# Performance work log

Measured on AMD Instinct MI355X. Metric: run time of the kernel, lower is better.

Reference implementation:

```python
import jax, jax.numpy as jnp
import numpy as np

N = 50000
F_DIM = 128
H_DIM = 128
E = 800000


def setup_inputs() -> dict:
    key = jax.random.key(0)
    ks = jax.random.split(key, 8)
    x = jax.random.normal(ks[0], (N, F_DIM), dtype=jnp.float32)
    edge_weight = jax.random.uniform(ks[1], (E,), dtype=jnp.float32)
    src = jax.random.randint(ks[2], (E,), 0, N)
    dst = jax.random.randint(ks[3], (E,), 0, N)
    edge_index = jnp.stack([src, dst]).astype(jnp.int64)
    sc = 1.0 / np.sqrt(F_DIM)
    W1 = jax.random.normal(ks[4], (F_DIM, H_DIM), dtype=jnp.float32) * sc
    W2 = jax.random.normal(ks[5], (H_DIM, H_DIM), dtype=jnp.float32) * sc
    Wfc = jax.random.normal(ks[6], (H_DIM, F_DIM), dtype=jnp.float32) * sc
    b1 = jnp.zeros((H_DIM,), jnp.float32)
    b2 = jnp.zeros((H_DIM,), jnp.float32)
    bfc = jnp.zeros((F_DIM,), jnp.float32)
    return {"x": x, "edge_weight": edge_weight, "W1": W1, "b1": b1,
            "W2": W2, "b2": b2, "Wfc": Wfc, "bfc": bfc,
            "edge_index": edge_index}


def _gcn_norm(src, dst, edge_weight, num_nodes):
    # PyG gcn_norm: add self-loops (weight 1), symmetric D^-1/2 A D^-1/2
    loop = jnp.arange(num_nodes, dtype=src.dtype)
    src2 = jnp.concatenate([src, loop])
    dst2 = jnp.concatenate([dst, loop])
    w2 = jnp.concatenate([edge_weight, jnp.ones((num_nodes,), edge_weight.dtype)])
    deg = jax.ops.segment_sum(w2, dst2, num_segments=num_nodes)
    dinv = jnp.where(deg > 0, jax.lax.rsqrt(jnp.where(deg > 0, deg, 1.0)), 0.0)
    norm = dinv[src2] * w2 * dinv[dst2]
    return src2, dst2, norm


def _gcn_conv(x, W, b, src, dst, norm, num_nodes):
    h = x @ W                              # [N, out]
    msg = norm[:, None] * h[src]           # gather + scale, [E+N, out]
    agg = jax.ops.segment_sum(msg, dst, num_segments=num_nodes)
    return agg + b


def reference(x, edge_weight, W1, b1, W2, b2, Wfc, bfc, edge_index):
    src, dst = edge_index[0], edge_index[1]
    src2, dst2, norm = _gcn_norm(src, dst, edge_weight, N)
    h = jax.nn.relu(_gcn_conv(x, W1, b1, src2, dst2, norm, N))
    h = jax.nn.relu(_gcn_conv(h, W2, b2, src2, dst2, norm, N))
    return h @ Wfc + bfc
```

## Files before the change

### kernel.cpp

```cpp
#include <hip/hip_runtime.h>
#include <hip/hip_fp16.h>


typedef unsigned long long u64;
typedef _Float16 f16x8 __attribute__((ext_vector_type(8)));
typedef float f32x4 __attribute__((ext_vector_type(4)));

#define CAP 96
#define CREG 5120

__global__ __launch_bounds__(256) void k_pre(unsigned* gcur,
                                             const float* __restrict__ W1,
                                             const float* __restrict__ W2,
                                             const float* __restrict__ Wfc,
                                             __half* __restrict__ Wt) {
    int i = blockIdx.x * 256 + threadIdx.x;
    if (i < 256) gcur[i] = 0u;
    if (i < 3 * 16384) {
        int w = i >> 14, r = i & 16383;
        int nn = r >> 7, kk = r & 127;
        const float* W = (w == 0) ? W1 : (w == 1) ? W2 : Wfc;
        Wt[i] = __float2half(W[kk * 128 + nn]);
    }
}

template <bool IN_FP32, bool OUT_HALF>
__device__ __forceinline__ void gemm_body(int bx, const void* __restrict__ Xv,
                                          const __half* __restrict__ Wt,
                                          const float* __restrict__ bias,
                                          void* __restrict__ Yv, int n) {
    __shared__ __align__(16) _Float16 Ws[128][136];
    int t = threadIdx.x;
    for (int i = t; i < 2048; i += 256) {
        int r = i >> 4, c8 = (i & 15) << 3;
        *(f16x8*)&Ws[r][c8] = *(const f16x8*)((const _Float16*)Wt + r * 128 + c8);
    }
    __syncthreads();

    int wave = t >> 6, lane = t & 63;
    int quad = lane >> 4, fcol = lane & 15;
    int rowbase = bx * 64 + wave * 16;
    int arow = rowbase + fcol;

    f16x8 a[4];
#pragma unroll
    for (int c = 0; c < 4; c++) {
        int k0 = c * 32 + quad * 8;
        if (arow < n) {
            if (IN_FP32) {
                const float* p = (const float*)Xv + (size_t)arow * 128 + k0;
#pragma unroll
                for (int j = 0; j < 8; j++) a[c][j] = (_Float16)p[j];
            } else {
                a[c] = *(const f16x8*)((const _Float16*)Xv + (size_t)arow * 128 + k0);
            }
        } else {
            f16x8 z = {0, 0, 0, 0, 0, 0, 0, 0};
            a[c] = z;
        }
    }

    f32x4 acc[8];
#pragma unroll
    for (int c = 0; c < 8; c++) acc[c] = (f32x4){0.f, 0.f, 0.f, 0.f};

#pragma unroll
    for (int kc = 0; kc < 4; kc++) {
        int k0 = kc * 32 + quad * 8;
#pragma unroll
        for (int ct = 0; ct < 8; ct++) {
            f16x8 b = *(const f16x8*)&Ws[ct * 16 + fcol][k0];
            acc[ct] = __builtin_amdgcn_mfma_f32_16x16x32_f16(a[kc], b, acc[ct], 0, 0, 0);
        }
    }

#pragma unroll
    for (int reg = 0; reg < 4; reg++) {
        int gr = rowbase + quad * 4 + reg;
        if (gr < n) {
            if (OUT_HALF) {
                __half* Y = (__half*)Yv;
#pragma unroll
                for (int ct = 0; ct < 8; ct++)
                    Y[(size_t)gr * 128 + ct * 16 + fcol] = __float2half(acc[ct][reg]);
            } else {
                float* Y = (float*)Yv;
#pragma unroll
                for (int ct = 0; ct < 8; ct++)
                    Y[(size_t)gr * 128 + ct * 16 + fcol] = acc[ct][reg] + bias[ct * 16 + fcol];
            }
        }
    }
}

template <bool IN_FP32, bool OUT_HALF>
__global__ __launch_bounds__(256) void k_gemm(const void* __restrict__ Xv,
                                              const __half* __restrict__ Wt,
                                              const float* __restrict__ bias,
                                              void* __restrict__ Yv, int n) {
    gemm_body<IN_FP32, OUT_HALF>(blockIdx.x, Xv, Wt, bias, Yv, n);
}

__device__ __forceinline__ void gemm1_body_nolds(int bx,
                                                 const float* __restrict__ X,
                                                 const __half* __restrict__ Wt,
                                                 __half* __restrict__ Y, int n) {
    int t = threadIdx.x;
    int wave = t >> 6, lane = t & 63;
    int quad = lane >> 4, fcol = lane & 15;
    int rowbase = bx * 64 + wave * 16;
    int arow = rowbase + fcol;

    f16x8 a[4];
#pragma unroll
    for (int c = 0; c < 4; c++) {
        int k0 = c * 32 + quad * 8;
        if (arow < n) {
            const float* p = X + (size_t)arow * 128 + k0;
#pragma unroll
            for (int j = 0; j < 8; j++) a[c][j] = (_Float16)p[j];
        } else {
            f16x8 z = {0, 0, 0, 0, 0, 0, 0, 0};
            a[c] = z;
        }
    }

    f32x4 acc[8];
#pragma unroll
    for (int c = 0; c < 8; c++) acc[c] = (f32x4){0.f, 0.f, 0.f, 0.f};

#pragma unroll
    for (int kc = 0; kc < 4; kc++) {
        int k0 = kc * 32 + quad * 8;
#pragma unroll
        for (int ct = 0; ct < 8; ct++) {
            f16x8 b = *(const f16x8*)((const _Float16*)Wt +
                                      (size_t)(ct * 16 + fcol) * 128 + k0);
            acc[ct] = __builtin_amdgcn_mfma_f32_16x16x32_f16(a[kc], b, acc[ct], 0, 0, 0);
        }
    }

#pragma unroll
    for (int reg = 0; reg < 4; reg++) {
        int gr = rowbase + quad * 4 + reg;
        if (gr < n) {
#pragma unroll
            for (int ct = 0; ct < 8; ct++)
                Y[(size_t)gr * 128 + ct * 16 + fcol] = __float2half(acc[ct][reg]);
        }
    }
}

__device__ __forceinline__ void p1_body(int bx, const int* __restrict__ src,
                                        const int* __restrict__ dst,
                                        const float* __restrict__ ew,
                                        unsigned* __restrict__ gcur,
                                        u64* __restrict__ coarse, int E, int NB) {
    __shared__ unsigned lcb[256];
    int t = threadIdx.x;
    lcb[t] = 0u;
    __syncthreads();

    u64 rec[16];
    unsigned br[16];
    int e0 = bx * 4096 + t;
#pragma unroll
    for (int k = 0; k < 16; k++) {
        int e = e0 + k * 256;
        if (e < E) {
            int d = dst[e];
            int s = src[e];
            unsigned wb = __float_as_uint(ew[e]);
            int bin = d >> 8;
            unsigned r = atomicAdd(&lcb[bin], 1u);
            rec[k] = ((u64)wb << 32) | ((u64)((unsigned)s << 8)) | (u64)(d & 255);
            br[k] = ((unsigned)bin << 16) | r;
        } else {
            br[k] = 0xFFFFFFFFu;
        }
    }
    __syncthreads();
    if (t < NB) {
        unsigned c = lcb[t];
        unsigned base = c ? atomicAdd(&gcur[t], c) : 0u;
        lcb[t] = base;
    }
    __syncthreads();
#pragma unroll
    for (int k = 0; k < 16; k++) {
        if (br[k] != 0xFFFFFFFFu) {
            int bin = br[k] >> 16;
            unsigned pos = lcb[bin] + (br[k] & 0xFFFFu);
            if (pos < CREG)
                coarse[(size_t)bin * CREG + pos] = rec[k];
        }
    }
}

__global__ __launch_bounds__(256) void k_gemm1_p1(
    const float* __restrict__ x, const __half* __restrict__ Wt,
    __half* __restrict__ bufH, int n, int GB,
    const int* __restrict__ src, const int* __restrict__ dst,
    const float* __restrict__ ew, unsigned* __restrict__ gcur,
    u64* __restrict__ coarse, int E, int NB) {
    int bx = blockIdx.x;
    if (bx < GB) {
        gemm1_body_nolds(bx, x, Wt, bufH, n);
        return;
    }
    p1_body(bx - GB, src, dst, ew, gcur, coarse, E, NB);
}

__global__ __launch_bounds__(256) void k_build(const u64* __restrict__ coarse,
                                               const unsigned* __restrict__ gcur,
                                               int2* __restrict__ slots,
                                               unsigned* __restrict__ cnt,
                                               float* __restrict__ dinv,
                                               int n) {
    __shared__ unsigned lcnt[256];
    __shared__ float lws[256];
    int b = blockIdx.x, t = threadIdx.x;
    lcnt[t] = 0u;
    lws[t] = 0.f;
    __syncthreads();
    int ec = min((int)gcur[b], CREG);
    const u64* reg = coarse + (size_t)b * CREG;
    int nb0 = b << 8;
    for (int e = t; e < ec; e += 256) {
        u64 r = reg[e];
        int dloc = (int)(r & 255u);
        int s = (int)((r >> 8) & 0xFFFFu);
        unsigned wb = (unsigned)(r >> 32);
        unsigned pos = atomicAdd(&lcnt[dloc], 1u);
        atomicAdd(&lws[dloc], __uint_as_float(wb));
        if (pos < CAP)
            slots[(size_t)(nb0 + dloc) * CAP + pos] = make_int2(s, (int)wb);
    }
    __syncthreads();
    int node = nb0 + t;
    if (node < n) {
        cnt[node] = lcnt[t];
        dinv[node] = rsqrtf(1.0f + lws[t]);
    }
}

__global__ __launch_bounds__(256) void k_agg(const __half* __restrict__ H,
                                             const int2* __restrict__ slots,
                                             const unsigned* __restrict__ cnt,
                                             const float* __restrict__ dinv,
                                             const float* __restrict__ bias,
                                             __half* __restrict__ out, int n) {
    int wid = (blockIdx.x * 256 + threadIdx.x) >> 6;
    int lane = threadIdx.x & 63;
    if (wid >= n) return;
    int i = __builtin_amdgcn_readfirstlane(wid);
    int c32 = lane & 31, hi = lane >> 5;
    float di = dinv[i];

    float acc0 = 0.f, acc1 = 0.f, acc2 = 0.f, acc3 = 0.f;
    {
        uint2 q = ((const uint2*)(H + (size_t)i * 128))[c32];
        float2 f0 = __half22float2(*(__half2*)&q.x);
        float2 f1 = __half22float2(*(__half2*)&q.y);
        if (hi == 0) {
            float dd = di * di;
            acc0 = dd * f0.x; acc1 = dd * f0.y;
            acc2 = dd * f1.x; acc3 = dd * f1.y;
        }
    }
    int c = min((int)cnt[i], CAP);
    const int2* row = slots + (size_t)i * CAP;

    for (int base = 0; base < c; base += 64) {
        int cnt2 = min(64, c - base);
        int mys = 0; float myv = 0.f;
        if (lane < cnt2) {
            int2 pr = row[base + lane];
            mys = pr.x;
            myv = dinv[pr.x] * __int_as_float(pr.y) * di;
        }
        int j = 0;
        for (; j + 16 <= cnt2; j += 16) {
            uint2 q[8]; float vv[8];
#pragma unroll
            for (int u = 0; u < 8; u++) {
                int s0 = __shfl(mys, j + 2 * u);
                int s1 = __shfl(mys, j + 2 * u + 1);
                float v0 = __shfl(myv, j + 2 * u);
                float v1 = __shfl(myv, j + 2 * u + 1);
                int s = hi ? s1 : s0;
                vv[u] = hi ? v1 : v0;
                q[u] = ((const uint2*)(H + (size_t)s * 128))[c32];
            }
#pragma unroll
            for (int u = 0; u < 8; u++) {
                float2 f0 = __half22float2(*(__half2*)&q[u].x);
                float2 f1 = __half22float2(*(__half2*)&q[u].y);
                acc0 = fmaf(vv[u], f0.x, acc0);
                acc1 = fmaf(vv[u], f0.y, acc1);
                acc2 = fmaf(vv[u], f1.x, acc2);
                acc3 = fmaf(vv[u], f1.y, acc3);
            }
        }
        for (; j < cnt2; j += 8) {
            uint2 q[4]; float vv[4];
#pragma unroll
            for (int u = 0; u < 4; u++) {
                int i0 = j + 2 * u, i1 = i0 + 1;
                int l0 = min(i0, cnt2 - 1), l1 = min(i1, cnt2 - 1);
                int s0 = __shfl(mys, l0);
                int s1 = __shfl(mys, l1);
                float v0 = __shfl(myv, l0);
                float v1 = __shfl(myv, l1);
                v0 = (i0 < cnt2) ? v0 : 0.f;
                v1 = (i1 < cnt2) ? v1 : 0.f;
                int s = hi ? s1 : s0;
                vv[u] = hi ? v1 : v0;
                q[u] = ((const uint2*)(H + (size_t)s * 128))[c32];
            }
#pragma unroll
            for (int u = 0; u < 4; u++) {
                float2 f0 = __half22float2(*(__half2*)&q[u].x);
                float2 f1 = __half22float2(*(__half2*)&q[u].y);
                acc0 = fmaf(vv[u], f0.x, acc0);
                acc1 = fmaf(vv[u], f0.y, acc1);
                acc2 = fmaf(vv[u], f1.x, acc2);
                acc3 = fmaf(vv[u], f1.y, acc3);
            }
        }
    }
    acc0 += __shfl_xor(acc0, 32);
    acc1 += __shfl_xor(acc1, 32);
    acc2 += __shfl_xor(acc2, 32);
    acc3 += __shfl_xor(acc3, 32);
    if (hi == 0) {
        float4 b4 = ((const float4*)bias)[c32];
        acc0 = fmaxf(acc0 + b4.x, 0.f);
        acc1 = fmaxf(acc1 + b4.y, 0.f);
        acc2 = fmaxf(acc2 + b4.z, 0.f);
        acc3 = fmaxf(acc3 + b4.w, 0.f);
        uint2 o;
        *(__half2*)&o.x = __floats2half2_rn(acc0, acc1);
        *(__half2*)&o.y = __floats2half2_rn(acc2, acc3);
        ((uint2*)(out + (size_t)i * 128))[c32] = o;
    }
}

extern "C" void kernel_launch(void* const* d_in, const int* in_sizes, int n_in,
                              void* d_out, int out_size, void* d_ws, size_t ws_size,
                              hipStream_t stream) {
    const float* x   = (const float*)d_in[0];
    const float* ew  = (const float*)d_in[1];
    const float* W1  = (const float*)d_in[2];
    const float* b1  = (const float*)d_in[3];
    const float* W2  = (const float*)d_in[4];
    const float* b2  = (const float*)d_in[5];
    const float* Wfc = (const float*)d_in[6];
    const float* bfc = (const float*)d_in[7];
    const int* eidx  = (const int*)d_in[8];

    const int E = in_sizes[1];
    const int N = in_sizes[0] / 128;
    const int* src = eidx;
    const int* dst = eidx + E;

    char* ws = (char*)d_ws;
    size_t off = 0;
    auto alloc = [&](size_t bytes) -> void* {
        void* p = ws + off;
        off = (off + bytes + 255) & ~(size_t)255;
        return p;
    };
    int gb  = (N + 63) / 64;
    int p1b = (E + 4095) / 4096;
    int NB  = (N + 255) >> 8;
    int ab  = (N * 64 + 255) / 256;
    int pb  = (3 * 16384 + 255) / 256;
    int Npad = N + 64;

    unsigned* gcur = (unsigned*)alloc(256 * 4);
    unsigned* cnt  = (unsigned*)alloc((size_t)N * 4);
    float*  dinv   = (float*)alloc((size_t)N * 4);
    u64*    coarse = (u64*)alloc((size_t)NB * CREG * 8);
    int2*   slots  = (int2*)alloc((size_t)N * CAP * 8);
    __half* Wt     = (__half*)alloc((size_t)3 * 16384 * 2);
    __half* bufH   = (__half*)alloc((size_t)Npad * 128 * 2);
    __half* bufA   = (__half*)alloc((size_t)Npad * 128 * 2);

    k_pre<<<pb, 256, 0, stream>>>(gcur, W1, W2, Wfc, Wt);
    k_gemm1_p1<<<gb + p1b, 256, 0, stream>>>(x, Wt, bufH, N, gb,
                                             src, dst, ew, gcur, coarse, E, NB);
    k_build<<<NB, 256, 0, stream>>>(coarse, gcur, slots, cnt, dinv, N);

    k_agg<<<ab, 256, 0, stream>>>(bufH, slots, cnt, dinv, b1, bufA, N);
    k_gemm<false, true><<<gb, 256, 0, stream>>>(bufA, Wt + 16384, nullptr, bufH, N);
    k_agg<<<ab, 256, 0, stream>>>(bufH, slots, cnt, dinv, b2, bufA, N);
    k_gemm<false, false><<<gb, 256, 0, stream>>>(bufA, Wt + 2 * 16384, bfc, d_out, N);
}
```

Measured before the change: 211.5 us.

## Split hidden features into four 32-column planes and aggregate per plane

```diff
diff --git a/kernel.cpp b/kernel.cpp
--- a/kernel.cpp
+++ b/kernel.cpp
@@ -24,11 +24,11 @@
     }
 }
 
-template <bool IN_FP32, bool OUT_HALF>
-__device__ __forceinline__ void gemm_body(int bx, const void* __restrict__ Xv,
+template <bool OUT_PLANES>
+__device__ __forceinline__ void gemm_body(int bx, const __half* __restrict__ Xp,
                                           const __half* __restrict__ Wt,
                                           const float* __restrict__ bias,
-                                          void* __restrict__ Yv, int n) {
+                                          void* __restrict__ Yv, int n, size_t PS) {
     __shared__ __align__(16) _Float16 Ws[128][136];
     int t = threadIdx.x;
     for (int i = t; i < 2048; i += 256) {
@@ -45,15 +45,9 @@
     f16x8 a[4];
 #pragma unroll
     for (int c = 0; c < 4; c++) {
-        int k0 = c * 32 + quad * 8;
         if (arow < n) {
-            if (IN_FP32) {
-                const float* p = (const float*)Xv + (size_t)arow * 128 + k0;
-#pragma unroll
-                for (int j = 0; j < 8; j++) a[c][j] = (_Float16)p[j];
-            } else {
-                a[c] = *(const f16x8*)((const _Float16*)Xv + (size_t)arow * 128 + k0);
-            }
+            a[c] = *(const f16x8*)((const _Float16*)Xp + c * PS +
+                                   (size_t)arow * 32 + quad * 8);
         } else {
             f16x8 z = {0, 0, 0, 0, 0, 0, 0, 0};
             a[c] = z;
@@ -78,11 +72,12 @@
     for (int reg = 0; reg < 4; reg++) {
         int gr = rowbase + quad * 4 + reg;
         if (gr < n) {
-            if (OUT_HALF) {
+            if (OUT_PLANES) {
                 __half* Y = (__half*)Yv;
 #pragma unroll
                 for (int ct = 0; ct < 8; ct++)
-                    Y[(size_t)gr * 128 + ct * 16 + fcol] = __float2half(acc[ct][reg]);
+                    Y[(ct >> 1) * PS + (size_t)gr * 32 + (ct & 1) * 16 + fcol] =
+                        __float2half(acc[ct][reg]);
             } else {
                 float* Y = (float*)Yv;
 #pragma unroll
@@ -93,18 +88,19 @@
     }
 }
 
-template <bool IN_FP32, bool OUT_HALF>
-__global__ __launch_bounds__(256) void k_gemm(const void* __restrict__ Xv,
+template <bool OUT_PLANES>
+__global__ __launch_bounds__(256) void k_gemm(const __half* __restrict__ Xp,
                                               const __half* __restrict__ Wt,
                                               const float* __restrict__ bias,
-                                              void* __restrict__ Yv, int n) {
-    gemm_body<IN_FP32, OUT_HALF>(blockIdx.x, Xv, Wt, bias, Yv, n);
+                                              void* __restrict__ Yv, int n, size_t PS) {
+    gemm_body<OUT_PLANES>(blockIdx.x, Xp, Wt, bias, Yv, n, PS);
 }
 
 __device__ __forceinline__ void gemm1_body_nolds(int bx,
                                                  const float* __restrict__ X,
                                                  const __half* __restrict__ Wt,
-                                                 __half* __restrict__ Y, int n) {
+                                                 __half* __restrict__ Y, int n,
+                                                 size_t PS) {
     int t = threadIdx.x;
     int wave = t >> 6, lane = t & 63;
     int quad = lane >> 4, fcol = lane & 15;
@@ -146,7 +142,8 @@
         if (gr < n) {
 #pragma unroll
             for (int ct = 0; ct < 8; ct++)
-                Y[(size_t)gr * 128 + ct * 16 + fcol] = __float2half(acc[ct][reg]);
+                Y[(ct >> 1) * PS + (size_t)gr * 32 + (ct & 1) * 16 + fcol] =
+                    __float2half(acc[ct][reg]);
         }
     }
 }
@@ -202,10 +199,10 @@
     __half* __restrict__ bufH, int n, int GB,
     const int* __restrict__ src, const int* __restrict__ dst,
     const float* __restrict__ ew, unsigned* __restrict__ gcur,
-    u64* __restrict__ coarse, int E, int NB) {
+    u64* __restrict__ coarse, int E, int NB, size_t PS) {
     int bx = blockIdx.x;
     if (bx < GB) {
-        gemm1_body_nolds(bx, x, Wt, bufH, n);
+        gemm1_body_nolds(bx, x, Wt, bufH, n, PS);
         return;
     }
     p1_body(bx - GB, src, dst, ew, gcur, coarse, E, NB);
@@ -244,29 +241,27 @@
     }
 }
 
-__global__ __launch_bounds__(256) void k_agg(const __half* __restrict__ H,
+__global__ __launch_bounds__(256) void k_agg(const __half* __restrict__ Hin,
                                              const int2* __restrict__ slots,
                                              const unsigned* __restrict__ cnt,
                                              const float* __restrict__ dinv,
                                              const float* __restrict__ bias,
-                                             __half* __restrict__ out, int n) {
-    int wid = (blockIdx.x * 256 + threadIdx.x) >> 6;
-    int lane = threadIdx.x & 63;
-    if (wid >= n) return;
-    int i = __builtin_amdgcn_readfirstlane(wid);
+                                             __half* __restrict__ Hout, int n,
+                                             size_t PS) {
+    int b = blockIdx.x;
+    int chunk = b & 3;
+    int wave = threadIdx.x >> 6, lane = threadIdx.x & 63;
+    int i = (b >> 2) * 4 + wave;
+    if (i >= n) return;
+    i = __builtin_amdgcn_readfirstlane(i);
     int c32 = lane & 31, hi = lane >> 5;
+    const __half* P = Hin + (size_t)chunk * PS;
     float di = dinv[i];
 
-    float acc0 = 0.f, acc1 = 0.f, acc2 = 0.f, acc3 = 0.f;
+    float acc = 0.f;
     {
-        uint2 q = ((const uint2*)(H + (size_t)i * 128))[c32];
-        float2 f0 = __half22float2(*(__half2*)&q.x);
-        float2 f1 = __half22float2(*(__half2*)&q.y);
-        if (hi == 0) {
-            float dd = di * di;
-            acc0 = dd * f0.x; acc1 = dd * f0.y;
-            acc2 = dd * f1.x; acc3 = dd * f1.y;
-        }
+        float h = __half2float(P[(size_t)i * 32 + c32]);
+        if (hi == 0) acc = di * di * h;
     }
     int c = min((int)cnt[i], CAP);
     const int2* row = slots + (size_t)i * CAP;
@@ -281,7 +276,7 @@
         }
         int j = 0;
         for (; j + 16 <= cnt2; j += 16) {
-            uint2 q[8]; float vv[8];
+            __half q[8]; float vv[8];
 #pragma unroll
             for (int u = 0; u < 8; u++) {
                 int s0 = __shfl(mys, j + 2 * u);
@@ -290,20 +285,14 @@
                 float v1 = __shfl(myv, j + 2 * u + 1);
                 int s = hi ? s1 : s0;
                 vv[u] = hi ? v1 : v0;
-                q[u] = ((const uint2*)(H + (size_t)s * 128))[c32];
+                q[u] = P[(size_t)s * 32 + c32];
             }
 #pragma unroll
-            for (int u = 0; u < 8; u++) {
-                float2 f0 = __half22float2(*(__half2*)&q[u].x);
-                float2 f1 = __half22float2(*(__half2*)&q[u].y);
-                acc0 = fmaf(vv[u], f0.x, acc0);
-                acc1 = fmaf(vv[u], f0.y, acc1);
-                acc2 = fmaf(vv[u], f1.x, acc2);
-                acc3 = fmaf(vv[u], f1.y, acc3);
-            }
+            for (int u = 0; u < 8; u++)
+                acc = fmaf(vv[u], __half2float(q[u]), acc);
         }
         for (; j < cnt2; j += 8) {
-            uint2 q[4]; float vv[4];
+            __half q[4]; float vv[4];
 #pragma unroll
             for (int u = 0; u < 4; u++) {
                 int i0 = j + 2 * u, i1 = i0 + 1;
@@ -316,33 +305,18 @@
                 v1 = (i1 < cnt2) ? v1 : 0.f;
                 int s = hi ? s1 : s0;
                 vv[u] = hi ? v1 : v0;
-                q[u] = ((const uint2*)(H + (size_t)s * 128))[c32];
+                q[u] = P[(size_t)s * 32 + c32];
             }
 #pragma unroll
-            for (int u = 0; u < 4; u++) {
-                float2 f0 = __half22float2(*(__half2*)&q[u].x);
-                float2 f1 = __half22float2(*(__half2*)&q[u].y);
-                acc0 = fmaf(vv[u], f0.x, acc0);
-                acc1 = fmaf(vv[u], f0.y, acc1);
-                acc2 = fmaf(vv[u], f1.x, acc2);
-                acc3 = fmaf(vv[u], f1.y, acc3);
-            }
-        }
-    }
-    acc0 += __shfl_xor(acc0, 32);
-    acc1 += __shfl_xor(acc1, 32);
-    acc2 += __shfl_xor(acc2, 32);
-    acc3 += __shfl_xor(acc3, 32);
+            for (int u = 0; u < 4; u++)
+                acc = fmaf(vv[u], __half2float(q[u]), acc);
+        }
+    }
+    acc += __shfl_xor(acc, 32);
     if (hi == 0) {
-        float4 b4 = ((const float4*)bias)[c32];
-        acc0 = fmaxf(acc0 + b4.x, 0.f);
-        acc1 = fmaxf(acc1 + b4.y, 0.f);
-        acc2 = fmaxf(acc2 + b4.z, 0.f);
-        acc3 = fmaxf(acc3 + b4.w, 0.f);
-        uint2 o;
-        *(__half2*)&o.x = __floats2half2_rn(acc0, acc1);
-        *(__half2*)&o.y = __floats2half2_rn(acc2, acc3);
-        ((uint2*)(out + (size_t)i * 128))[c32] = o;
+        float bb = bias[chunk * 32 + c32];
+        acc = fmaxf(acc + bb, 0.f);
+        Hout[(size_t)chunk * PS + (size_t)i * 32 + c32] = __float2half(acc);
     }
 }
 
@@ -374,9 +348,10 @@
     int gb  = (N + 63) / 64;
     int p1b = (E + 4095) / 4096;
     int NB  = (N + 255) >> 8;
-    int ab  = (N * 64 + 255) / 256;
+    int ab  = 4 * ((N + 3) / 4);
     int pb  = (3 * 16384 + 255) / 256;
     int Npad = N + 64;
+    size_t PS = (size_t)Npad * 32;
 
     unsigned* gcur = (unsigned*)alloc(256 * 4);
     unsigned* cnt  = (unsigned*)alloc((size_t)N * 4);
@@ -384,16 +359,16 @@
     u64*    coarse = (u64*)alloc((size_t)NB * CREG * 8);
     int2*   slots  = (int2*)alloc((size_t)N * CAP * 8);
     __half* Wt     = (__half*)alloc((size_t)3 * 16384 * 2);
-    __half* bufH   = (__half*)alloc((size_t)Npad * 128 * 2);
-    __half* bufA   = (__half*)alloc((size_t)Npad * 128 * 2);
+    __half* bufH   = (__half*)alloc(PS * 4 * 2);
+    __half* bufA   = (__half*)alloc(PS * 4 * 2);
 
     k_pre<<<pb, 256, 0, stream>>>(gcur, W1, W2, Wfc, Wt);
     k_gemm1_p1<<<gb + p1b, 256, 0, stream>>>(x, Wt, bufH, N, gb,
-                                             src, dst, ew, gcur, coarse, E, NB);
+                                             src, dst, ew, gcur, coarse, E, NB, PS);
     k_build<<<NB, 256, 0, stream>>>(coarse, gcur, slots, cnt, dinv, N);
 
-    k_agg<<<ab, 256, 0, stream>>>(bufH, slots, cnt, dinv, b1, bufA, N);
-    k_gemm<false, true><<<gb, 256, 0, stream>>>(bufA, Wt + 16384, nullptr, bufH, N);
-    k_agg<<<ab, 256, 0, stream>>>(bufH, slots, cnt, dinv, b2, bufA, N);
-    k_gemm<false, false><<<gb, 256, 0, stream>>>(bufA, Wt + 2 * 16384, bfc, d_out, N);
-}
+    k_agg<<<ab, 256, 0, stream>>>(bufH, slots, cnt, dinv, b1, bufA, N, PS);
+    k_gemm<true><<<gb, 256, 0, stream>>>(bufA, Wt + 16384, nullptr, bufH, N, PS);
+    k_agg<<<ab, 256, 0, stream>>>(bufH, slots, cnt, dinv, b2, bufA, N, PS);
+    k_gemm<false><<<gb, 256, 0, stream>>>(bufA, Wt + 2 * 16384, bfc, d_out, N, PS);
+}
```

After: 315.7 us. 1.49x slower.
